# Kernel optimization log

Measured on AMD Instinct MI355X. Metric: run time of the kernel, lower is better.

The kernel has to match this reference:

```python
import jax, jax.numpy as jnp
import numpy as np

E = 8      # n_routed_experts (== n_local)
K = 2      # n_activated_experts (top-k)
DIM = 2048
INTER = 1408
N_SHARED = 2
STD = 0.02


def setup_inputs() -> dict:
    key = jax.random.key(0)
    ks = jax.random.split(key, 9)
    B, S = 2, 2048
    return {
        "x": jax.random.normal(ks[0], (B, S, DIM), dtype=jnp.float32),
        "gate_w": jax.random.normal(ks[1], (E, DIM), dtype=jnp.float32) * STD,
        "router_bias": jnp.zeros((E,), dtype=jnp.float32),
        "W1": jax.random.normal(ks[2], (E, DIM, INTER), dtype=jnp.float32) * STD,
        "W3": jax.random.normal(ks[3], (E, DIM, INTER), dtype=jnp.float32) * STD,
        "W2": jax.random.normal(ks[4], (E, INTER, DIM), dtype=jnp.float32) * STD,
        "sw1": jax.random.normal(ks[5], (N_SHARED * INTER, DIM), dtype=jnp.float32) * STD,
        "sw3": jax.random.normal(ks[6], (N_SHARED * INTER, DIM), dtype=jnp.float32) * STD,
        "sw2": jax.random.normal(ks[7], (DIM, N_SHARED * INTER), dtype=jnp.float32) * STD,
    }


def reference(x, gate_w, router_bias, W1, W3, W2, sw1, sw3, sw2):
    B, S, D = x.shape
    X = x.reshape(-1, D)                       # [T, D]
    T = X.shape[0]

    # ---- Router: sigmoid scores, biased top-k selection, normalized weights
    logits = jnp.einsum('td,ed->te', X, gate_w)          # [T, E] (route_scale == 1.0)
    scores = jax.nn.sigmoid(logits)
    sel = scores + router_bias[None, :]
    _, idx = jax.lax.top_k(sel, K)                       # [T, K] int indices
    w = jnp.take_along_axis(scores, idx, axis=1)         # gather true scores
    w = w / jnp.clip(jnp.sum(w, axis=-1, keepdims=True), 1e-12)

    # Dense combine matrix [T, E]: gate weight where expert selected else 0
    gate_full = jnp.zeros((T, E), dtype=w.dtype).at[jnp.arange(T)[:, None], idx].set(w)

    # ---- Expert MLPs (SwiGLU) computed per-expert, combined by routing weight
    h1 = jnp.einsum('td,edh->eth', X, W1)                # [E, T, INTER]
    h3 = jnp.einsum('td,edh->eth', X, W3)
    y = jnp.einsum('eth,ehd->etd', jax.nn.silu(h1) * h3, W2)  # [E, T, D]
    out = jnp.einsum('etd,te->td', y, gate_full)         # weighted combine

    # ---- Shared expert MLP (always on)
    shared = jnp.einsum('th,dh->td',
                        jax.nn.silu(jnp.einsum('td,hd->th', X, sw1))
                        * jnp.einsum('td,hd->th', X, sw3), sw2)
    out = out + shared
    return out.reshape(B, S, D)
```

## Files before the change

kernel.cpp:

```cpp
#include <hip/hip_runtime.h>

#define DEV __device__ __forceinline__

typedef __attribute__((ext_vector_type(8))) short short8;
typedef __attribute__((ext_vector_type(4))) float floatx4;

constexpr int Tn  = 4096;
constexpr int Dm  = 2048;
constexpr int In  = 1408;
constexpr int En  = 8;
constexpr int SIn = 2816;
constexpr int CAP = 9216;

constexpr int RT_H = (CAP / 128) * (In / 128);
constexpr int SH_H = (Tn / 128) * (SIn / 128);
constexpr int RT_O = (CAP / 128) * (Dm / 128);
constexpr int SH_O = (Tn / 128) * (Dm / 128);

DEV unsigned short f2bf(float f) {
  unsigned int u = __float_as_uint(f);
  u += 0x7FFF + ((u >> 16) & 1);
  return (unsigned short)(u >> 16);
}

DEV float bf2f(unsigned short u) {
  return __uint_as_float(((unsigned int)u) << 16);
}

DEV void gl2lds16(const unsigned short* g, unsigned short* l) {
  __builtin_amdgcn_global_load_lds(
      (const __attribute__((address_space(1))) unsigned int*)g,
      (__attribute__((address_space(3))) unsigned int*)l, 16, 0, 0);
}

DEV int fragaddr(int row, int chunk) {
  return row * 64 + ((chunk ^ (row & 7)) * 8);
}


__global__ void convert_all_kernel(const float* __restrict__ x,
                                   const float* __restrict__ sw1,
                                   const float* __restrict__ sw3,
                                   const float* __restrict__ sw2,
                                   unsigned short* __restrict__ Xb,
                                   unsigned short* __restrict__ sw1b,
                                   unsigned short* __restrict__ sw3b,
                                   unsigned short* __restrict__ sw2b) {
  int y = blockIdx.y;
  const float* src; unsigned short* dst; int n4;
  if (y == 0)      { src = x;   dst = Xb;   n4 = Tn * Dm / 4; }
  else if (y == 1) { src = sw1; dst = sw1b; n4 = SIn * Dm / 4; }
  else if (y == 2) { src = sw3; dst = sw3b; n4 = SIn * Dm / 4; }
  else             { src = sw2; dst = sw2b; n4 = Dm * SIn / 4; }
  int i = blockIdx.x * 256 + threadIdx.x;
  if (i >= n4) return;
  float4 v = ((const float4*)src)[i];
  union { unsigned short u[4]; unsigned long long ll; } p;
  p.u[0] = f2bf(v.x); p.u[1] = f2bf(v.y); p.u[2] = f2bf(v.z); p.u[3] = f2bf(v.w);
  *(unsigned long long*)(dst + (long)i * 4) = p.ll;
}

__global__ void transpose_all_kernel(const float* __restrict__ W1,
                                     const float* __restrict__ W3,
                                     const float* __restrict__ W2,
                                     unsigned short* __restrict__ W1t,
                                     unsigned short* __restrict__ W3t,
                                     unsigned short* __restrict__ W2t) {
  __shared__ float tile[32][33];
  int z = blockIdx.z;
  const float* s0; unsigned short* d0; int R, C;
  if (z == 0)      { s0 = W1; d0 = W1t; R = Dm; C = In; }
  else if (z == 1) { s0 = W3; d0 = W3t; R = Dm; C = In; }
  else             { s0 = W2; d0 = W2t; R = In; C = Dm; }
  int tilesC = C >> 5;
  int tr = (blockIdx.x / tilesC) << 5;
  int tc = (blockIdx.x % tilesC) << 5;
  const float* s = s0 + (long)blockIdx.y * R * C;
  unsigned short* d = d0 + (long)blockIdx.y * R * C;
  int tx = threadIdx.x & 31, ty = threadIdx.x >> 5;
#pragma unroll
  for (int i = 0; i < 4; i++)
    tile[ty + 8 * i][tx] = s[(long)(tr + ty + 8 * i) * C + tc + tx];
  __syncthreads();
#pragma unroll
  for (int i = 0; i < 4; i++)
    d[(long)(tc + ty + 8 * i) * R + tr + tx] = f2bf(tile[tx][ty + 8 * i]);
}


__global__ void init_kernel(int* counts, int* ptok) {
  int i = blockIdx.x * 256 + threadIdx.x;
  if (i < En) counts[i] = 0;
  if (i < CAP) ptok[i] = 0;
}

__global__ void router_kernel(const float* __restrict__ X, const float* __restrict__ GW,
                              const float* __restrict__ bias,
                              int* __restrict__ route_e, float* __restrict__ route_w,
                              int* __restrict__ counts) {
  int t = blockIdx.x, lane = threadIdx.x;
  const float* xr = X + (long)t * Dm;
  double acc[En];
#pragma unroll
  for (int e = 0; e < En; e++) acc[e] = 0.0;
  for (int d = lane; d < Dm; d += 64) {
    double xv = (double)xr[d];
#pragma unroll
    for (int e = 0; e < En; e++) acc[e] += xv * (double)GW[e * Dm + d];
  }
#pragma unroll
  for (int off = 32; off > 0; off >>= 1) {
#pragma unroll
    for (int e = 0; e < En; e++) acc[e] += __shfl_down(acc[e], off);
  }
  if (lane == 0) {
    double sc[En], sel[En];
#pragma unroll
    for (int e = 0; e < En; e++) {
      sc[e] = 1.0 / (1.0 + exp(-acc[e]));
      sel[e] = sc[e] + (double)bias[e];
    }
    int i0 = 0;
#pragma unroll
    for (int e = 1; e < En; e++) if (sel[e] > sel[i0]) i0 = e;
    int i1 = (i0 == 0) ? 1 : 0;
#pragma unroll
    for (int e = 0; e < En; e++) if (e != i0 && sel[e] > sel[i1]) i1 = e;
    double s = sc[i0] + sc[i1];
    if (s < 1e-12) s = 1e-12;
    route_e[t * 2] = i0;  route_e[t * 2 + 1] = i1;
    route_w[t * 2] = (float)(sc[i0] / s);  route_w[t * 2 + 1] = (float)(sc[i1] / s);
    atomicAdd(&counts[i0], 1);  atomicAdd(&counts[i1], 1);
  }
}

__global__ void offsets_kernel(const int* __restrict__ counts,
                               int* __restrict__ offs, int* __restrict__ fill) {
  if (threadIdx.x == 0) {
    int off = 0;
    for (int e = 0; e < En; e++) {
      offs[e] = off; fill[e] = off;
      off += (counts[e] + 127) & ~127;
    }
    offs[En] = off;
  }
}

__global__ void scatter_kernel(const int* __restrict__ re, int* __restrict__ fill,
                               int* __restrict__ pt, int* __restrict__ pslot) {
  int i = blockIdx.x * 256 + threadIdx.x;
  if (i < Tn * 2) {
    int e = re[i];
    int slot = atomicAdd(&fill[e], 1);
    pt[slot] = i >> 1;
    pslot[i] = slot;
  }
}


__global__ __launch_bounds__(256, 2)
void h_gemm_all(const unsigned short* __restrict__ Xb,
                const unsigned short* __restrict__ W1t,
                const unsigned short* __restrict__ W3t,
                const unsigned short* __restrict__ sw1b,
                const unsigned short* __restrict__ sw3b,
                unsigned short* __restrict__ act,
                unsigned short* __restrict__ actS,
                const int* __restrict__ ptok,
                const int* __restrict__ offs) {
  __shared__ unsigned short sA[128 * 64];
  __shared__ unsigned short sB1[128 * 64];
  __shared__ unsigned short sB3[128 * 64];
  const int Kd = Dm;
  int bid = blockIdx.x;
  bool routed = bid < RT_H;
  int m0, n0, N;
  const unsigned short *B1p, *B3p;
  unsigned short* ap;
  if (routed) {
    m0 = (bid % 72) * 128; n0 = (bid / 72) * 128;
    if (m0 >= offs[En]) return;
    int e = 0;
    while (!(m0 >= offs[e] && m0 < offs[e + 1])) e++;
    B1p = W1t + (long)e * In * Dm;
    B3p = W3t + (long)e * In * Dm;
    ap = act; N = In;
  } else {
    int b2 = bid - RT_H;
    m0 = (b2 % 32) * 128; n0 = (b2 / 32) * 128;
    B1p = sw1b; B3p = sw3b;
    ap = actS; N = SIn;
  }
  int tid = threadIdx.x, wave = tid >> 6, lane = tid & 63;
  int lr = lane >> 3, lc = lane & 7;
  int lcs = lc ^ lr;
  const unsigned short *gA[4], *gB1[4], *gB3[4];
#pragma unroll
  for (int j = 0; j < 4; j++) {
    int r = wave * 32 + j * 8 + lr;
    long arow = routed ? (long)ptok[m0 + r] : (long)(m0 + r);
    gA[j]  = Xb  + arow * Kd + lcs * 8;
    gB1[j] = B1p + (long)(n0 + r) * Kd + lcs * 8;
    gB3[j] = B3p + (long)(n0 + r) * Kd + lcs * 8;
  }
  int wm = wave >> 1, wn = wave & 1;
  int fr = lane & 15, fq = lane >> 4;
  floatx4 acc1[4][4], acc3[4][4];
#pragma unroll
  for (int mi = 0; mi < 4; mi++)
#pragma unroll
    for (int ni = 0; ni < 4; ni++) { acc1[mi][ni] = (floatx4)0.0f; acc3[mi][ni] = (floatx4)0.0f; }

  for (int k0 = 0; k0 < Kd; k0 += 64) {
    __syncthreads();
#pragma unroll
    for (int j = 0; j < 4; j++) {
      int rb = (wave * 32 + j * 8) * 64;
      gl2lds16(gA[j]  + k0, &sA[rb]);
      gl2lds16(gB1[j] + k0, &sB1[rb]);
      gl2lds16(gB3[j] + k0, &sB3[rb]);
    }
    __syncthreads();
#pragma unroll
    for (int kk = 0; kk < 2; kk++) {
      short8 af[4], b1f[4], b3f[4];
#pragma unroll
      for (int i = 0; i < 4; i++) {
        af[i]  = *(const short8*)&sA [fragaddr(wm * 64 + i * 16 + fr, kk * 4 + fq)];
        b1f[i] = *(const short8*)&sB1[fragaddr(wn * 64 + i * 16 + fr, kk * 4 + fq)];
        b3f[i] = *(const short8*)&sB3[fragaddr(wn * 64 + i * 16 + fr, kk * 4 + fq)];
      }
#pragma unroll
      for (int mi = 0; mi < 4; mi++)
#pragma unroll
        for (int ni = 0; ni < 4; ni++) {
          acc1[mi][ni] = __builtin_amdgcn_mfma_f32_16x16x32_bf16(af[mi], b1f[ni], acc1[mi][ni], 0, 0, 0);
          acc3[mi][ni] = __builtin_amdgcn_mfma_f32_16x16x32_bf16(af[mi], b3f[ni], acc3[mi][ni], 0, 0, 0);
        }
    }
  }
#pragma unroll
  for (int mi = 0; mi < 4; mi++)
#pragma unroll
    for (int ni = 0; ni < 4; ni++)
#pragma unroll
      for (int r = 0; r < 4; r++) {
        int row = m0 + wm * 64 + mi * 16 + fq * 4 + r;
        int col = n0 + wn * 64 + ni * 16 + fr;
        float h1 = acc1[mi][ni][r], h3 = acc3[mi][ni][r];
        float v = h1 / (1.0f + __expf(-h1)) * h3;
        ap[(long)row * N + col] = f2bf(v);
      }
}


__global__ __launch_bounds__(256, 2)
void o_gemm_all(const unsigned short* __restrict__ act,
                const unsigned short* __restrict__ actS,
                const unsigned short* __restrict__ W2t,
                const unsigned short* __restrict__ sw2b,
                unsigned short* __restrict__ yR,
                float* __restrict__ out,
                const int* __restrict__ offs) {
  __shared__ unsigned short sA[128 * 64];
  __shared__ unsigned short sB[128 * 64];
  int bid = blockIdx.x;
  bool routed = bid < RT_O;
  int m0, n0, Kd;
  const unsigned short *Ap, *Bp;
  if (routed) {
    m0 = (bid % 72) * 128; n0 = (bid / 72) * 128;
    if (m0 >= offs[En]) return;
    int e = 0;
    while (!(m0 >= offs[e] && m0 < offs[e + 1])) e++;
    Ap = act; Bp = W2t + (long)e * Dm * In; Kd = In;
  } else {
    int b2 = bid - RT_O;
    m0 = (b2 % 32) * 128; n0 = (b2 / 32) * 128;
    Ap = actS; Bp = sw2b; Kd = SIn;
  }
  int tid = threadIdx.x, wave = tid >> 6, lane = tid & 63;
  int lr = lane >> 3, lc = lane & 7;
  int lcs = lc ^ lr;
  const unsigned short *gA[4], *gB[4];
#pragma unroll
  for (int j = 0; j < 4; j++) {
    int r = wave * 32 + j * 8 + lr;
    gA[j] = Ap + (long)(m0 + r) * Kd + lcs * 8;
    gB[j] = Bp + (long)(n0 + r) * Kd + lcs * 8;
  }
  int wm = wave >> 1, wn = wave & 1;
  int fr = lane & 15, fq = lane >> 4;
  floatx4 acc[4][4];
#pragma unroll
  for (int mi = 0; mi < 4; mi++)
#pragma unroll
    for (int ni = 0; ni < 4; ni++) acc[mi][ni] = (floatx4)0.0f;

  for (int k0 = 0; k0 < Kd; k0 += 64) {
    __syncthreads();
#pragma unroll
    for (int j = 0; j < 4; j++) {
      int rb = (wave * 32 + j * 8) * 64;
      gl2lds16(gA[j] + k0, &sA[rb]);
      gl2lds16(gB[j] + k0, &sB[rb]);
    }
    __syncthreads();
#pragma unroll
    for (int kk = 0; kk < 2; kk++) {
      short8 af[4], bf[4];
#pragma unroll
      for (int i = 0; i < 4; i++) {
        af[i] = *(const short8*)&sA[fragaddr(wm * 64 + i * 16 + fr, kk * 4 + fq)];
        bf[i] = *(const short8*)&sB[fragaddr(wn * 64 + i * 16 + fr, kk * 4 + fq)];
      }
#pragma unroll
      for (int mi = 0; mi < 4; mi++)
#pragma unroll
        for (int ni = 0; ni < 4; ni++)
          acc[mi][ni] = __builtin_amdgcn_mfma_f32_16x16x32_bf16(af[mi], bf[ni], acc[mi][ni], 0, 0, 0);
    }
  }
#pragma unroll
  for (int mi = 0; mi < 4; mi++)
#pragma unroll
    for (int r = 0; r < 4; r++) {
      int row = m0 + wm * 64 + mi * 16 + fq * 4 + r;
#pragma unroll
      for (int ni = 0; ni < 4; ni++) {
        int col = n0 + wn * 64 + ni * 16 + fr;
        if (routed) yR[(long)row * Dm + col] = f2bf(acc[mi][ni][r]);
        else        out[(long)row * Dm + col] = acc[mi][ni][r];
      }
    }
}


__global__ void combine_kernel(const unsigned short* __restrict__ yR,
                               const int* __restrict__ pslot,
                               const float* __restrict__ rw,
                               float* __restrict__ out) {
  int idx = blockIdx.x * 256 + threadIdx.x;
  int t = idx >> 9, c4 = idx & 511;
  int s0 = pslot[t * 2], s1 = pslot[t * 2 + 1];
  float w0 = rw[t * 2], w1 = rw[t * 2 + 1];
  ushort4 a = ((const ushort4*)(yR + (long)s0 * Dm))[c4];
  ushort4 b = ((const ushort4*)(yR + (long)s1 * Dm))[c4];
  float4* op = (float4*)(out + (long)t * Dm) + c4;
  float4 o = *op;
  o.x += w0 * bf2f(a.x) + w1 * bf2f(b.x);
  o.y += w0 * bf2f(a.y) + w1 * bf2f(b.y);
  o.z += w0 * bf2f(a.z) + w1 * bf2f(b.z);
  o.w += w0 * bf2f(a.w) + w1 * bf2f(b.w);
  *op = o;
}


extern "C" void kernel_launch(void* const* d_in, const int* in_sizes, int n_in,
                              void* d_out, int out_size, void* d_ws, size_t ws_size,
                              hipStream_t stream) {
  const float* x    = (const float*)d_in[0];
  const float* gw   = (const float*)d_in[1];
  const float* bias = (const float*)d_in[2];
  const float* W1   = (const float*)d_in[3];
  const float* W3   = (const float*)d_in[4];
  const float* W2   = (const float*)d_in[5];
  const float* sw1  = (const float*)d_in[6];
  const float* sw3  = (const float*)d_in[7];
  const float* sw2  = (const float*)d_in[8];
  float* out = (float*)d_out;

  char* p = (char*)d_ws;
  auto alloc = [&](size_t bytes) {
    char* r = p; p += (bytes + 255) & ~(size_t)255; return r;
  };
  unsigned short* Xb   = (unsigned short*)alloc((size_t)Tn * Dm * 2);
  unsigned short* W1t  = (unsigned short*)alloc((size_t)En * In * Dm * 2);
  unsigned short* W3t  = (unsigned short*)alloc((size_t)En * In * Dm * 2);
  unsigned short* W2t  = (unsigned short*)alloc((size_t)En * Dm * In * 2);
  unsigned short* sw1b = (unsigned short*)alloc((size_t)SIn * Dm * 2);
  unsigned short* sw3b = (unsigned short*)alloc((size_t)SIn * Dm * 2);
  unsigned short* sw2b = (unsigned short*)alloc((size_t)Dm * SIn * 2);
  unsigned short* act  = (unsigned short*)alloc((size_t)CAP * In * 2);
  unsigned short* actS = (unsigned short*)alloc((size_t)Tn * SIn * 2);
  unsigned short* yR   = (unsigned short*)alloc((size_t)CAP * Dm * 2);
  int*   route_e = (int*)alloc(Tn * 2 * 4);
  float* route_w = (float*)alloc(Tn * 2 * 4);
  int*   counts  = (int*)alloc(256);
  int*   offs    = (int*)alloc(256);
  int*   fill    = (int*)alloc(256);
  int*   ptok    = (int*)alloc(CAP * 4);
  int*   pslot   = (int*)alloc(Tn * 2 * 4);

  convert_all_kernel<<<dim3(Tn * Dm / 4 / 256, 4), 256, 0, stream>>>(
      x, sw1, sw3, sw2, Xb, sw1b, sw3b, sw2b);
  transpose_all_kernel<<<dim3((Dm / 32) * (In / 32), En, 3), 256, 0, stream>>>(
      W1, W3, W2, W1t, W3t, W2t);

  init_kernel<<<(CAP + 255) / 256, 256, 0, stream>>>(counts, ptok);
  router_kernel<<<Tn, 64, 0, stream>>>(x, gw, bias, route_e, route_w, counts);
  offsets_kernel<<<1, 1, 0, stream>>>(counts, offs, fill);
  scatter_kernel<<<Tn * 2 / 256, 256, 0, stream>>>(route_e, fill, ptok, pslot);

  h_gemm_all<<<RT_H + SH_H, 256, 0, stream>>>(
      Xb, W1t, W3t, sw1b, sw3b, act, actS, ptok, offs);
  o_gemm_all<<<RT_O + SH_O, 256, 0, stream>>>(
      act, actS, W2t, sw2b, yR, out, offs);
  combine_kernel<<<Tn * (Dm / 4) / 256, 256, 0, stream>>>(yR, pslot, route_w, out);
}
```

Before: 864.1 us.

## Rewrite MoE GEMMs as 256x256 tiles with double-buffered LDS pipeline

Replaces the 128x128, 256-thread GEMM kernels with a shared 256x256-tile core run by 512 threads. The core uses 128KB of dynamic LDS, double-buffered so global-to-LDS loads for the next K-tiles overlap MFMA work, with explicit waitcnt, barriers and setprio interleaving. W1 and W3 are merged into one B tile for the gate/up GEMM. Expert padding and capacity rise to 256-row granularity, which adds wasted rows per expert. The larger tiles cut the number of blocks, which may leave parts of the GPU idle.

```diff
diff --git a/kernel.cpp b/kernel.cpp
--- a/kernel.cpp
+++ b/kernel.cpp
@@ -10,12 +10,12 @@
 constexpr int In  = 1408;
 constexpr int En  = 8;
 constexpr int SIn = 2816;
-constexpr int CAP = 9216;
-
-constexpr int RT_H = (CAP / 128) * (In / 128);
-constexpr int SH_H = (Tn / 128) * (SIn / 128);
-constexpr int RT_O = (CAP / 128) * (Dm / 128);
-constexpr int SH_O = (Tn / 128) * (Dm / 128);
+constexpr int CAP = 10240;
+
+constexpr int RT_H = (CAP / 256) * (In / 128);
+constexpr int SH_H = (Tn / 256) * (SIn / 128);
+constexpr int RT_O = (CAP / 256) * (Dm / 256);
+constexpr int SH_O = (Tn / 256) * (Dm / 256);
 
 DEV unsigned short f2bf(float f) {
   unsigned int u = __float_as_uint(f);
@@ -27,15 +27,18 @@
   return __uint_as_float(((unsigned int)u) << 16);
 }
 
-DEV void gl2lds16(const unsigned short* g, unsigned short* l) {
+DEV void stg(const char* g, char* l) {
   __builtin_amdgcn_global_load_lds(
       (const __attribute__((address_space(1))) unsigned int*)g,
       (__attribute__((address_space(3))) unsigned int*)l, 16, 0, 0);
 }
 
-DEV int fragaddr(int row, int chunk) {
-  return row * 64 + ((chunk ^ (row & 7)) * 8);
-}
+#define BARR()  __builtin_amdgcn_s_barrier()
+#define LGKM0() do { asm volatile("s_waitcnt lgkmcnt(0)" ::: "memory"); \
+                     __builtin_amdgcn_sched_barrier(0); } while (0)
+#define LGKM8() asm volatile("s_waitcnt lgkmcnt(8)" ::: "memory")
+#define VMC(n)  asm volatile("s_waitcnt vmcnt(" #n ")" ::: "memory")
+#define PRIO(x) __builtin_amdgcn_s_setprio(x)
 
 
 __global__ void convert_all_kernel(const float* __restrict__ x,
@@ -140,7 +143,7 @@
     int off = 0;
     for (int e = 0; e < En; e++) {
       offs[e] = off; fill[e] = off;
-      off += (counts[e] + 127) & ~127;
+      off += (counts[e] + 255) & ~255;
     }
     offs[En] = off;
   }
@@ -158,7 +161,93 @@
 }
 
 
-__global__ __launch_bounds__(256, 2)
+DEV void rdA(short8 (&af)[4][2], const char* Ard, int m0i) {
+#pragma unroll
+  for (int i = 0; i < 4; i++)
+#pragma unroll
+    for (int kk = 0; kk < 2; kk++)
+      af[i][kk] = *(const short8*)(Ard + (((m0i + i) * 2 + kk) << 10));
+}
+
+DEV void rdB(short8 (&bf)[4][2], const char* Brd, int n0i) {
+#pragma unroll
+  for (int n = 0; n < 2; n++)
+#pragma unroll
+    for (int kk = 0; kk < 2; kk++)
+      bf[n0i + n][kk] = *(const short8*)(Brd + (((n0i + n) * 2 + kk) << 10));
+}
+
+DEV void mm16(floatx4 (&acc)[8][4], const short8 (&af)[4][2],
+              const short8 (&bf)[4][2], int mq, int nq) {
+#pragma unroll
+  for (int i = 0; i < 4; i++)
+#pragma unroll
+    for (int n = 0; n < 2; n++)
+#pragma unroll
+      for (int kk = 0; kk < 2; kk++)
+        acc[4 * mq + i][2 * nq + n] = __builtin_amdgcn_mfma_f32_16x16x32_bf16(
+            af[i][kk], bf[2 * nq + n][kk], acc[4 * mq + i][2 * nq + n], 0, 0, 0);
+}
+
+DEV void chunk_rc(int c, int& rowh, int& colb) {
+  rowh = ((c >> 7) << 4) | ((c >> 2) & 15);
+  colb = (((c >> 6) & 1) << 6) | ((((c & 3) << 4)) ^ ((c & 32) ? 32 : 0));
+}
+
+DEV void gemm_core(char* LDS, const char* (&gA)[2][2], const char* (&gB)[2][2],
+                   floatx4 (&acc)[8][4], int NT, int wm, int wn, int wv, int aswz) {
+  const int bsel = (wn >> 1) * 16384 + ((wn & 1) << 13);
+  const int wb = wv * 1024;
+  stg(gB[0][0], LDS + 32768 + wb);
+  stg(gB[1][0], LDS + 32768 + 16384 + wb);
+  stg(gB[0][1], LDS + 32768 + 8192 + wb);
+  stg(gB[1][1], LDS + 32768 + 16384 + 8192 + wb);
+  stg(gA[0][0], LDS + wb);
+  stg(gA[1][0], LDS + 16384 + wb);
+  stg(gA[0][1], LDS + 8192 + wb);
+  stg(gA[1][1], LDS + 16384 + 8192 + wb);
+  stg(gA[0][0] + 128, LDS + 65536 + wb);
+  stg(gA[1][0] + 128, LDS + 65536 + 16384 + wb);
+  stg(gB[0][0] + 128, LDS + 65536 + 32768 + wb);
+  stg(gB[1][0] + 128, LDS + 65536 + 32768 + 16384 + wb);
+  VMC(4);
+  BARR();
+  short8 af[4][2], bf[4][2];
+
+  auto tile = [&](int t, int b) {
+    const char* Ard = LDS + (b << 16) + wm * 16384 + aswz;
+    const char* Brd = LDS + (b << 16) + 32768 + bsel + aswz;
+    char* An = LDS + ((b ^ 1) << 16);
+    char* Bn = An + 32768;
+    char* Ac = LDS + (b << 16);
+    char* Bc = Ac + 32768;
+    const int kn = (t + 1) << 7, ka = (t + 2) << 7;
+    const bool s1 = (t + 1 < NT), s2 = (t + 2 < NT);
+    rdA(af, Ard, 0); rdB(bf, Brd, 0);
+    if (s1) { stg(gB[0][1] + kn, Bn + 8192 + wb);
+              stg(gB[1][1] + kn, Bn + 16384 + 8192 + wb); }
+    LGKM8(); BARR(); LGKM0(); PRIO(1); mm16(acc, af, bf, 0, 0); PRIO(0); BARR();
+    rdB(bf, Brd, 2);
+    if (s1) { stg(gA[0][1] + kn, An + 8192 + wb);
+              stg(gA[1][1] + kn, An + 16384 + 8192 + wb); }
+    BARR(); LGKM0(); PRIO(1); mm16(acc, af, bf, 0, 1); PRIO(0); BARR();
+    rdA(af, Ard, 4);
+    if (s2) { stg(gA[0][0] + ka, Ac + wb);
+              stg(gA[1][0] + ka, Ac + 16384 + wb); }
+    BARR(); LGKM0(); PRIO(1); mm16(acc, af, bf, 1, 0); PRIO(0); BARR();
+    if (s2) { stg(gB[0][0] + ka, Bc + wb);
+              stg(gB[1][0] + ka, Bc + 16384 + wb); }
+    BARR(); LGKM0(); PRIO(1); mm16(acc, af, bf, 1, 1); PRIO(0);
+    if (s2)      { VMC(4); }
+    else if (s1) { VMC(0); }
+    BARR();
+  };
+#pragma unroll 1
+  for (int t2 = 0; t2 < NT; t2 += 2) { tile(t2, 0); tile(t2 + 1, 1); }
+}
+
+
+__global__ __launch_bounds__(512, 2)
 void h_gemm_all(const unsigned short* __restrict__ Xb,
                 const unsigned short* __restrict__ W1t,
                 const unsigned short* __restrict__ W3t,
@@ -168,93 +257,71 @@
                 unsigned short* __restrict__ actS,
                 const int* __restrict__ ptok,
                 const int* __restrict__ offs) {
-  __shared__ unsigned short sA[128 * 64];
-  __shared__ unsigned short sB1[128 * 64];
-  __shared__ unsigned short sB3[128 * 64];
-  const int Kd = Dm;
+  extern __shared__ char LDS[];
   int bid = blockIdx.x;
   bool routed = bid < RT_H;
-  int m0, n0, N;
+  int m0, n0, Nact;
   const unsigned short *B1p, *B3p;
   unsigned short* ap;
   if (routed) {
-    m0 = (bid % 72) * 128; n0 = (bid / 72) * 128;
+    m0 = (bid % 40) * 256; n0 = (bid / 40) * 128;
     if (m0 >= offs[En]) return;
     int e = 0;
     while (!(m0 >= offs[e] && m0 < offs[e + 1])) e++;
     B1p = W1t + (long)e * In * Dm;
     B3p = W3t + (long)e * In * Dm;
-    ap = act; N = In;
+    ap = act; Nact = In;
   } else {
     int b2 = bid - RT_H;
-    m0 = (b2 % 32) * 128; n0 = (b2 / 32) * 128;
+    m0 = (b2 % 16) * 256; n0 = (b2 / 16) * 128;
     B1p = sw1b; B3p = sw3b;
-    ap = actS; N = SIn;
-  }
-  int tid = threadIdx.x, wave = tid >> 6, lane = tid & 63;
-  int lr = lane >> 3, lc = lane & 7;
-  int lcs = lc ^ lr;
-  const unsigned short *gA[4], *gB1[4], *gB3[4];
-#pragma unroll
-  for (int j = 0; j < 4; j++) {
-    int r = wave * 32 + j * 8 + lr;
-    long arow = routed ? (long)ptok[m0 + r] : (long)(m0 + r);
-    gA[j]  = Xb  + arow * Kd + lcs * 8;
-    gB1[j] = B1p + (long)(n0 + r) * Kd + lcs * 8;
-    gB3[j] = B3p + (long)(n0 + r) * Kd + lcs * 8;
-  }
-  int wm = wave >> 1, wn = wave & 1;
+    ap = actS; Nact = SIn;
+  }
+  int tid = threadIdx.x, wv = tid >> 6, lane = tid & 63;
+  int wm = wv >> 2, wn = wv & 3;
   int fr = lane & 15, fq = lane >> 4;
-  floatx4 acc1[4][4], acc3[4][4];
-#pragma unroll
-  for (int mi = 0; mi < 4; mi++)
-#pragma unroll
-    for (int ni = 0; ni < 4; ni++) { acc1[mi][ni] = (floatx4)0.0f; acc3[mi][ni] = (floatx4)0.0f; }
-
-  for (int k0 = 0; k0 < Kd; k0 += 64) {
-    __syncthreads();
-#pragma unroll
-    for (int j = 0; j < 4; j++) {
-      int rb = (wave * 32 + j * 8) * 64;
-      gl2lds16(gA[j]  + k0, &sA[rb]);
-      gl2lds16(gB1[j] + k0, &sB1[rb]);
-      gl2lds16(gB3[j] + k0, &sB3[rb]);
+  int aswz = fr * 64 + ((fq * 16) ^ ((fr & 8) << 2));
+
+  const char* gA[2][2]; const char* gB[2][2];
+#pragma unroll
+  for (int j = 0; j < 2; j++) {
+    int rowh, colb;
+    chunk_rc(j * 512 + tid, rowh, colb);
+#pragma unroll
+    for (int h = 0; h < 2; h++) {
+      int grA = m0 + h * 128 + rowh;
+      long ra = routed ? (long)ptok[grA] : (long)grA;
+      gA[h][j] = (const char*)Xb + ra * (long)(Dm * 2) + colb;
+      int rt = h * 128 + rowh;
+      const unsigned short* src = ((rt >> 5) & 1) ? B3p : B1p;
+      long rb = (long)n0 + ((rt >> 6) << 5) + (rt & 31);
+      gB[h][j] = (const char*)src + rb * (long)(Dm * 2) + colb;
     }
-    __syncthreads();
-#pragma unroll
-    for (int kk = 0; kk < 2; kk++) {
-      short8 af[4], b1f[4], b3f[4];
-#pragma unroll
-      for (int i = 0; i < 4; i++) {
-        af[i]  = *(const short8*)&sA [fragaddr(wm * 64 + i * 16 + fr, kk * 4 + fq)];
-        b1f[i] = *(const short8*)&sB1[fragaddr(wn * 64 + i * 16 + fr, kk * 4 + fq)];
-        b3f[i] = *(const short8*)&sB3[fragaddr(wn * 64 + i * 16 + fr, kk * 4 + fq)];
+  }
+  floatx4 acc[8][4];
+#pragma unroll
+  for (int i = 0; i < 8; i++)
+#pragma unroll
+    for (int n = 0; n < 4; n++) acc[i][n] = (floatx4)0.0f;
+
+  gemm_core(LDS, gA, gB, acc, Dm / 64, wm, wn, wv, aswz);
+
+#pragma unroll
+  for (int mi = 0; mi < 8; mi++)
+#pragma unroll
+    for (int n = 0; n < 2; n++)
+#pragma unroll
+      for (int r = 0; r < 4; r++) {
+        int row = m0 + wm * 128 + mi * 16 + fq * 4 + r;
+        int col = n0 + wn * 32 + n * 16 + fr;
+        float h1 = acc[mi][n][r], h3 = acc[mi][n + 2][r];
+        float v = h1 / (1.0f + __expf(-h1)) * h3;
+        ap[(long)row * Nact + col] = f2bf(v);
       }
-#pragma unroll
-      for (int mi = 0; mi < 4; mi++)
-#pragma unroll
-        for (int ni = 0; ni < 4; ni++) {
-          acc1[mi][ni] = __builtin_amdgcn_mfma_f32_16x16x32_bf16(af[mi], b1f[ni], acc1[mi][ni], 0, 0, 0);
-          acc3[mi][ni] = __builtin_amdgcn_mfma_f32_16x16x32_bf16(af[mi], b3f[ni], acc3[mi][ni], 0, 0, 0);
-        }
-    }
-  }
-#pragma unroll
-  for (int mi = 0; mi < 4; mi++)
-#pragma unroll
-    for (int ni = 0; ni < 4; ni++)
-#pragma unroll
-      for (int r = 0; r < 4; r++) {
-        int row = m0 + wm * 64 + mi * 16 + fq * 4 + r;
-        int col = n0 + wn * 64 + ni * 16 + fr;
-        float h1 = acc1[mi][ni][r], h3 = acc3[mi][ni][r];
-        float v = h1 / (1.0f + __expf(-h1)) * h3;
-        ap[(long)row * N + col] = f2bf(v);
-      }
-}
-
-
-__global__ __launch_bounds__(256, 2)
+}
+
+
+__global__ __launch_bounds__(512, 2)
 void o_gemm_all(const unsigned short* __restrict__ act,
                 const unsigned short* __restrict__ actS,
                 const unsigned short* __restrict__ W2t,
@@ -262,70 +329,51 @@
                 unsigned short* __restrict__ yR,
                 float* __restrict__ out,
                 const int* __restrict__ offs) {
-  __shared__ unsigned short sA[128 * 64];
-  __shared__ unsigned short sB[128 * 64];
+  extern __shared__ char LDS[];
   int bid = blockIdx.x;
   bool routed = bid < RT_O;
-  int m0, n0, Kd;
-  const unsigned short *Ap, *Bp;
+  int m0, n0, lda, ldb, NT;
+  const unsigned short *Apt, *Bpt;
   if (routed) {
-    m0 = (bid % 72) * 128; n0 = (bid / 72) * 128;
+    m0 = (bid % 40) * 256; n0 = (bid / 40) * 256;
     if (m0 >= offs[En]) return;
     int e = 0;
     while (!(m0 >= offs[e] && m0 < offs[e + 1])) e++;
-    Ap = act; Bp = W2t + (long)e * Dm * In; Kd = In;
+    Apt = act; lda = In; Bpt = W2t + (long)e * Dm * In; ldb = In; NT = In / 64;
   } else {
     int b2 = bid - RT_O;
-    m0 = (b2 % 32) * 128; n0 = (b2 / 32) * 128;
-    Ap = actS; Bp = sw2b; Kd = SIn;
-  }
-  int tid = threadIdx.x, wave = tid >> 6, lane = tid & 63;
-  int lr = lane >> 3, lc = lane & 7;
-  int lcs = lc ^ lr;
-  const unsigned short *gA[4], *gB[4];
-#pragma unroll
-  for (int j = 0; j < 4; j++) {
-    int r = wave * 32 + j * 8 + lr;
-    gA[j] = Ap + (long)(m0 + r) * Kd + lcs * 8;
-    gB[j] = Bp + (long)(n0 + r) * Kd + lcs * 8;
-  }
-  int wm = wave >> 1, wn = wave & 1;
+    m0 = (b2 % 16) * 256; n0 = (b2 / 16) * 256;
+    Apt = actS; lda = SIn; Bpt = sw2b; ldb = SIn; NT = SIn / 64;
+  }
+  int tid = threadIdx.x, wv = tid >> 6, lane = tid & 63;
+  int wm = wv >> 2, wn = wv & 3;
   int fr = lane & 15, fq = lane >> 4;
-  floatx4 acc[4][4];
-#pragma unroll
-  for (int mi = 0; mi < 4; mi++)
-#pragma unroll
-    for (int ni = 0; ni < 4; ni++) acc[mi][ni] = (floatx4)0.0f;
-
-  for (int k0 = 0; k0 < Kd; k0 += 64) {
-    __syncthreads();
-#pragma unroll
-    for (int j = 0; j < 4; j++) {
-      int rb = (wave * 32 + j * 8) * 64;
-      gl2lds16(gA[j] + k0, &sA[rb]);
-      gl2lds16(gB[j] + k0, &sB[rb]);
+  int aswz = fr * 64 + ((fq * 16) ^ ((fr & 8) << 2));
+
+  const char* gA[2][2]; const char* gB[2][2];
+#pragma unroll
+  for (int j = 0; j < 2; j++) {
+    int rowh, colb;
+    chunk_rc(j * 512 + tid, rowh, colb);
+#pragma unroll
+    for (int h = 0; h < 2; h++) {
+      gA[h][j] = (const char*)Apt + (long)(m0 + h * 128 + rowh) * (lda * 2) + colb;
+      gB[h][j] = (const char*)Bpt + (long)(n0 + h * 128 + rowh) * (ldb * 2) + colb;
     }
-    __syncthreads();
-#pragma unroll
-    for (int kk = 0; kk < 2; kk++) {
-      short8 af[4], bf[4];
-#pragma unroll
-      for (int i = 0; i < 4; i++) {
-        af[i] = *(const short8*)&sA[fragaddr(wm * 64 + i * 16 + fr, kk * 4 + fq)];
-        bf[i] = *(const short8*)&sB[fragaddr(wn * 64 + i * 16 + fr, kk * 4 + fq)];
-      }
-#pragma unroll
-      for (int mi = 0; mi < 4; mi++)
-#pragma unroll
-        for (int ni = 0; ni < 4; ni++)
-          acc[mi][ni] = __builtin_amdgcn_mfma_f32_16x16x32_bf16(af[mi], bf[ni], acc[mi][ni], 0, 0, 0);
-    }
-  }
-#pragma unroll
-  for (int mi = 0; mi < 4; mi++)
+  }
+  floatx4 acc[8][4];
+#pragma unroll
+  for (int i = 0; i < 8; i++)
+#pragma unroll
+    for (int n = 0; n < 4; n++) acc[i][n] = (floatx4)0.0f;
+
+  gemm_core(LDS, gA, gB, acc, NT, wm, wn, wv, aswz);
+
+#pragma unroll
+  for (int mi = 0; mi < 8; mi++)
 #pragma unroll
     for (int r = 0; r < 4; r++) {
-      int row = m0 + wm * 64 + mi * 16 + fq * 4 + r;
+      int row = m0 + wm * 128 + mi * 16 + fq * 4 + r;
 #pragma unroll
       for (int ni = 0; ni < 4; ni++) {
         int col = n0 + wn * 64 + ni * 16 + fr;
@@ -369,6 +417,15 @@
   const float* sw3  = (const float*)d_in[7];
   const float* sw2  = (const float*)d_in[8];
   float* out = (float*)d_out;
+
+  static bool attr_done = false;
+  if (!attr_done) {
+    hipFuncSetAttribute(reinterpret_cast<const void*>(h_gemm_all),
+                        hipFuncAttributeMaxDynamicSharedMemorySize, 131072);
+    hipFuncSetAttribute(reinterpret_cast<const void*>(o_gemm_all),
+                        hipFuncAttributeMaxDynamicSharedMemorySize, 131072);
+    attr_done = true;
+  }
 
   char* p = (char*)d_ws;
   auto alloc = [&](size_t bytes) {
@@ -402,9 +459,9 @@
   offsets_kernel<<<1, 1, 0, stream>>>(counts, offs, fill);
   scatter_kernel<<<Tn * 2 / 256, 256, 0, stream>>>(route_e, fill, ptok, pslot);
 
-  h_gemm_all<<<RT_H + SH_H, 256, 0, stream>>>(
+  h_gemm_all<<<RT_H + SH_H, 512, 131072, stream>>>(
       Xb, W1t, W3t, sw1b, sw3b, act, actS, ptok, offs);
-  o_gemm_all<<<RT_O + SH_O, 256, 0, stream>>>(
+  o_gemm_all<<<RT_O + SH_O, 512, 131072, stream>>>(
       act, actS, W2t, sw2b, yR, out, offs);
   combine_kernel<<<Tn * (Dm / 4) / 256, 256, 0, stream>>>(yR, pslot, route_w, out);
 }
```

Result: no change. 870.6 us (+0.7%).
